# Kernel tuning notes

Measured on AMD Instinct MI355X. Metric: run time of the kernel, lower is better.

The kernel has to match this reference:

```python
import jax, jax.numpy as jnp
import numpy as np

NH, NKV, HD = 32, 8, 128   # query heads, kv heads, head_dim
EPS = 1e-6
ROPE_BASE = 10000.0


def setup_inputs() -> dict:
    key = jax.random.key(0)
    ks = jax.random.split(key, 5)
    B, S, H = 2, 1024, 4096
    scale = 0.02
    return {
        "x": jax.random.normal(ks[0], (B, S, H), jnp.float32),
        "wq": jax.random.normal(ks[1], (H, NH * HD), jnp.float32) * scale,
        "wk": jax.random.normal(ks[2], (H, NKV * HD), jnp.float32) * scale,
        "wv": jax.random.normal(ks[3], (H, NKV * HD), jnp.float32) * scale,
        "wo": jax.random.normal(ks[4], (NH * HD, H), jnp.float32) * scale,
        "q_norm_w": jnp.ones((HD,), jnp.float32),
        "k_norm_w": jnp.ones((HD,), jnp.float32),
    }


def _rmsnorm(t, w):
    # per-head RMSNorm over last dim (head_dim)
    var = jnp.mean(t * t, axis=-1, keepdims=True)
    return t * jax.lax.rsqrt(var + EPS) * w


def _rope(t, cos, sin):
    # t: [B,S,h,d]; cos/sin: [S, d/2] (neox / rotate-half style)
    d2 = t.shape[-1] // 2
    t1, t2 = t[..., :d2], t[..., d2:]
    c = cos[None, :, None, :]
    s = sin[None, :, None, :]
    return jnp.concatenate([t1 * c - t2 * s, t1 * s + t2 * c], axis=-1)


def reference(x, wq, wk, wv, wo, q_norm_w, k_norm_w):
    B, S, H = x.shape
    softmax_scale = HD ** (-0.5)

    q = (x @ wq).reshape(B, S, NH, HD)
    k = (x @ wk).reshape(B, S, NKV, HD)
    v = (x @ wv).reshape(B, S, NKV, HD)

    # QK RMSNorm (qwen3 use_qk_norm)
    q = _rmsnorm(q, q_norm_w)
    k = _rmsnorm(k, k_norm_w)

    # rotary embedding, base 10000
    inv_freq = 1.0 / (ROPE_BASE ** (jnp.arange(0, HD, 2, dtype=jnp.float32) / HD))
    ang = jnp.arange(S, dtype=jnp.float32)[:, None] * inv_freq[None, :]  # [S, d/2]
    cos, sin = jnp.cos(ang), jnp.sin(ang)
    q = _rope(q, cos, sin)
    k = _rope(k, cos, sin)

    # GQA: expand kv heads to match query heads
    g = NH // NKV
    k = jnp.repeat(k, g, axis=2)  # [B,S,NH,HD]
    v = jnp.repeat(v, g, axis=2)

    scores = jnp.einsum("bqhd,bkhd->bhqk", q, k) * softmax_scale
    causal = jnp.tril(jnp.ones((S, S), dtype=bool))
    scores = jnp.where(causal[None, None], scores, jnp.finfo(scores.dtype).min)
    probs = jax.nn.softmax(scores, axis=-1)
    ctx = jnp.einsum("bhqk,bkhd->bqhd", probs, v).reshape(B, S, NH * HD)
    return ctx @ wo
```

## Files before the change

kernel.cpp:

```cpp
#include <hip/hip_runtime.h>


#define NH_ 32
#define NKV_ 8
#define HD_ 128
#define SEQ_ 1024
#define HID_ 4096
#define NQKV_ 6144

typedef unsigned short u16;
typedef __bf16 bf16x8 __attribute__((ext_vector_type(8)));
typedef float f32x4 __attribute__((ext_vector_type(4)));

__device__ __forceinline__ u16 f2bf(float f) {
  unsigned int u = __float_as_uint(f);
  return (u16)((u + 0x7FFFu + ((u >> 16) & 1u)) >> 16);
}
__device__ __forceinline__ float bf2f(u16 u) {
  return __uint_as_float(((unsigned int)u) << 16);
}
__device__ __forceinline__ f32x4 mfma16(bf16x8 a, bf16x8 b, f32x4 c) {
  return __builtin_amdgcn_mfma_f32_16x16x32_bf16(a, b, c, 0, 0, 0);
}
__device__ __forceinline__ void gld16(u16* lds, const u16* g) {
  __builtin_amdgcn_global_load_lds(
      (const __attribute__((address_space(1))) unsigned int*)g,
      (__attribute__((address_space(3))) unsigned int*)lds, 16, 0, 0);
}

__global__ __launch_bounds__(256) void cvt_bf16(const float* __restrict__ src,
                                                u16* __restrict__ dst) {
  int i = (blockIdx.x * 256 + threadIdx.x) * 8;
  float4 a = *(const float4*)(src + i);
  float4 b = *(const float4*)(src + i + 4);
  u16 o[8];
  o[0] = f2bf(a.x); o[1] = f2bf(a.y); o[2] = f2bf(a.z); o[3] = f2bf(a.w);
  o[4] = f2bf(b.x); o[5] = f2bf(b.y); o[6] = f2bf(b.z); o[7] = f2bf(b.w);
  *(uint4*)(dst + i) = *(uint4*)&o[0];
}

__global__ __launch_bounds__(256) void transpose_cvt(
    const float* __restrict__ src, int ldn, u16* __restrict__ dst, int K) {
  __shared__ float t[32][33];
  const int k0 = blockIdx.x * 32, n0 = blockIdx.y * 32;
  const int c = threadIdx.x & 31, r4 = threadIdx.x >> 5;
#pragma unroll
  for (int i = 0; i < 4; ++i) {
    int r = r4 + i * 8;
    t[r][c] = src[(size_t)(k0 + r) * ldn + n0 + c];
  }
  __syncthreads();
#pragma unroll
  for (int i = 0; i < 4; ++i) {
    int r = r4 + i * 8;
    dst[(size_t)(n0 + r) * K + k0 + c] = f2bf(t[c][r]);
  }
}

__global__ __launch_bounds__(256) void v_transpose(const u16* __restrict__ QKV,
                                                   u16* __restrict__ VT) {
  __shared__ u16 t[32][33];
  const int s0 = blockIdx.x * 32, d0 = blockIdx.y * 32;
  const int bkvh = blockIdx.z;
  const int b = bkvh >> 3, kvh = bkvh & 7;
  const int c = threadIdx.x & 31, r8 = threadIdx.x >> 5;
#pragma unroll
  for (int i = 0; i < 4; ++i) {
    int r = r8 + i * 8;
    t[r][c] = QKV[(size_t)(b * SEQ_ + s0 + r) * NQKV_ + 5120 + kvh * 128 + d0 + c];
  }
  __syncthreads();
#pragma unroll
  for (int i = 0; i < 4; ++i) {
    int r = r8 + i * 8;
    VT[(size_t)(bkvh * HD_ + d0 + r) * SEQ_ + s0 + c] = t[c][r];
  }
}

template <bool F32OUT>
__global__ __launch_bounds__(256) void gemm_bt(const u16* __restrict__ A,
                                               const u16* __restrict__ Bt,
                                               void* __restrict__ Cv, int K,
                                               int ldc) {
  __shared__ u16 As[128 * 32];
  __shared__ u16 Bs[128 * 32];
  const int bn = blockIdx.x, bm = blockIdx.y;
  const int tid = threadIdx.x, lane = tid & 63, w = tid >> 6;
  const int wr = w >> 1, wc = w & 1, ln = lane & 15, quad = lane >> 4;

  const int srow = w * 32 + (lane >> 2);
  const int skk = (lane & 3) * 8;
  const u16* ag = A + (size_t)(bm * 128 + srow) * K + skk;
  const u16* bg = Bt + (size_t)(bn * 128 + srow) * K + skk;
  u16* asd = &As[w * 1024];
  u16* bsd = &Bs[w * 1024];

  f32x4 acc[4][4];
#pragma unroll
  for (int i = 0; i < 4; ++i)
#pragma unroll
    for (int j = 0; j < 4; ++j)
#pragma unroll
      for (int r = 0; r < 4; ++r) acc[i][j][r] = 0.0f;

  for (int kb = 0; kb < K / 32; ++kb) {
    gld16(asd, ag);
    gld16(asd + 512, ag + 16 * (size_t)K);
    gld16(bsd, bg);
    gld16(bsd + 512, bg + 16 * (size_t)K);
    ag += 32;
    bg += 32;
    __syncthreads();
    bf16x8 af[4], bfr[4];
#pragma unroll
    for (int i = 0; i < 4; ++i)
      af[i] = *(const bf16x8*)&As[(wr * 64 + i * 16 + ln) * 32 + quad * 8];
#pragma unroll
    for (int j = 0; j < 4; ++j)
      bfr[j] = *(const bf16x8*)&Bs[(wc * 64 + j * 16 + ln) * 32 + quad * 8];
#pragma unroll
    for (int i = 0; i < 4; ++i)
#pragma unroll
      for (int j = 0; j < 4; ++j) acc[i][j] = mfma16(af[i], bfr[j], acc[i][j]);
    __syncthreads();
  }
#pragma unroll
  for (int i = 0; i < 4; ++i) {
#pragma unroll
    for (int r = 0; r < 4; ++r) {
      int grow = bm * 128 + wr * 64 + i * 16 + quad * 4 + r;
      int gcol = bn * 128 + wc * 64 + ln;
      if (F32OUT) {
        float* dst = (float*)Cv + (size_t)grow * ldc + gcol;
#pragma unroll
        for (int j = 0; j < 4; ++j) dst[j * 16] = acc[i][j][r];
      } else {
        u16* dst = (u16*)Cv + (size_t)grow * ldc + gcol;
#pragma unroll
        for (int j = 0; j < 4; ++j) dst[j * 16] = f2bf(acc[i][j][r]);
      }
    }
  }
}

__global__ __launch_bounds__(256) void norm_rope(
    const u16* __restrict__ QKV, const float* __restrict__ QW,
    const float* __restrict__ KW, u16* __restrict__ QB, u16* __restrict__ KB) {
  const float QSCALE = 0.08838834764831845f * 1.4426950408889634f;
  int vec = blockIdx.x * 4 + (threadIdx.x >> 6);
  int lane = threadIdx.x & 63;
  const u16* src;
  u16* dst;
  const float* nw;
  int m;
  float outsc;
  if (vec < 65536) {
    m = vec >> 5;
    int hh = vec & 31;
    src = QKV + (size_t)m * NQKV_ + hh * 128;
    int b = m >> 10, s = m & 1023;
    dst = QB + (size_t)((b * NH_ + hh) * SEQ_ + s) * HD_;
    nw = QW;
    outsc = QSCALE;
  } else {
    int vk = vec - 65536;
    m = vk >> 3;
    int kvh = vk & 7;
    src = QKV + (size_t)m * NQKV_ + 4096 + kvh * 128;
    int b = m >> 10, s = m & 1023;
    dst = KB + (size_t)((b * NKV_ + kvh) * SEQ_ + s) * HD_;
    nw = KW;
    outsc = 1.0f;
  }
  float t1 = bf2f(src[lane]), t2 = bf2f(src[lane + 64]);
  float ss = t1 * t1 + t2 * t2;
#pragma unroll
  for (int off = 32; off >= 1; off >>= 1) ss += __shfl_xor(ss, off);
  float scale = rsqrtf(ss * (1.0f / 128.0f) + 1e-6f) * outsc;
  float n1 = t1 * scale * nw[lane];
  float n2 = t2 * scale * nw[lane + 64];
  int spos = m & 1023;
  float invf = powf(10000.0f, -(float)lane * (1.0f / 64.0f));
  float ang = (float)spos * invf;
  float sn, cs;
  sincosf(ang, &sn, &cs);
  dst[lane] = f2bf(n1 * cs - n2 * sn);
  dst[lane + 64] = f2bf(n1 * sn + n2 * cs);
}

__global__ __launch_bounds__(256) void flash_attn(
    const u16* __restrict__ QB, const u16* __restrict__ KB,
    const u16* __restrict__ VT, u16* __restrict__ CTX) {
  __shared__ u16 Ks[4][64][32];
  __shared__ u16 Vs[2][128][32];
  __shared__ u16 Pl[4][16][72];

  const int bid = blockIdx.x;
  const int qt = 15 - (bid >> 6);
  const int h = bid & 31, b = (bid >> 5) & 1;
  const int kvh = h >> 2;
  const int tid = threadIdx.x, w = tid >> 6, lane = tid & 63;
  const int ln = lane & 15, quad = lane >> 4;
  const int l4 = lane >> 2, l4r = lane & 3;

  const u16* qbase =
      QB + (size_t)((b * NH_ + h) * SEQ_ + qt * 64 + w * 16 + ln) * HD_;
  bf16x8 qf[4];
#pragma unroll
  for (int kc = 0; kc < 4; ++kc)
    qf[kc] = *(const bf16x8*)(qbase + kc * 32 + quad * 8);

  f32x4 o[8];
#pragma unroll
  for (int t = 0; t < 8; ++t)
#pragma unroll
    for (int r = 0; r < 4; ++r) o[t][r] = 0.0f;
  float m_r[4] = {-3e38f, -3e38f, -3e38f, -3e38f};
  float l_r[4] = {0.0f, 0.0f, 0.0f, 0.0f};

  const u16* krow = KB + (size_t)((b * NKV_ + kvh) * SEQ_ + w * 16 + l4) * HD_ +
                    l4r * 8;
  const u16* vrow = VT + (size_t)((b * NKV_ + kvh) * HD_ + w * 32 + l4) * SEQ_ +
                    l4r * 8;
  const int pswz = ((ln >> 3) & 1) << 3;

  for (int kt = 0; kt <= qt; ++kt) {
    const int key0 = kt * 64;
#pragma unroll
    for (int i = 0; i < 4; ++i)
      gld16(&Ks[i][w * 16][0], krow + (size_t)key0 * HD_ + i * 32);
#pragma unroll
    for (int i = 0; i < 4; ++i)
      gld16(&Vs[i & 1][w * 32 + (i >> 1) * 16][0],
            vrow + (size_t)(i >> 1) * 16 * SEQ_ + key0 + (i & 1) * 32);
    __syncthreads();

    f32x4 sc[4];
#pragma unroll
    for (int t2 = 0; t2 < 4; ++t2) {
#pragma unroll
      for (int r = 0; r < 4; ++r) sc[t2][r] = 0.0f;
#pragma unroll
      for (int kc = 0; kc < 4; ++kc) {
        bf16x8 kf = *(const bf16x8*)&Ks[kc][t2 * 16 + ln][quad * 8];
        sc[t2] = mfma16(qf[kc], kf, sc[t2]);
      }
    }

    const bool diag = (kt == qt);
    float p[4][4], alpha[4];
#pragma unroll
    for (int r = 0; r < 4; ++r) {
      float s0 = sc[0][r], s1 = sc[1][r], s2 = sc[2][r], s3 = sc[3][r];
      if (diag) {
        const int qi = qt * 64 + w * 16 + quad * 4 + r;
        if (key0 + ln > qi) s0 = -3e38f;
        if (key0 + 16 + ln > qi) s1 = -3e38f;
        if (key0 + 32 + ln > qi) s2 = -3e38f;
        if (key0 + 48 + ln > qi) s3 = -3e38f;
      }
      float mx = fmaxf(fmaxf(s0, s1), fmaxf(s2, s3));
#pragma unroll
      for (int off = 1; off < 16; off <<= 1) mx = fmaxf(mx, __shfl_xor(mx, off));
      float mnew = fmaxf(m_r[r], mx);
      alpha[r] = exp2f(m_r[r] - mnew);
      p[0][r] = exp2f(s0 - mnew);
      p[1][r] = exp2f(s1 - mnew);
      p[2][r] = exp2f(s2 - mnew);
      p[3][r] = exp2f(s3 - mnew);
      float rs = p[0][r] + p[1][r] + p[2][r] + p[3][r];
#pragma unroll
      for (int off = 1; off < 16; off <<= 1) rs += __shfl_xor(rs, off);
      l_r[r] = l_r[r] * alpha[r] + rs;
      m_r[r] = mnew;
    }
#pragma unroll
    for (int t = 0; t < 8; ++t)
#pragma unroll
      for (int r = 0; r < 4; ++r) o[t][r] *= alpha[r];

#pragma unroll
    for (int r = 0; r < 4; ++r) {
      const int row = quad * 4 + r;
      const int wswz = ((row >> 3) & 1) << 3;
#pragma unroll
      for (int t2 = 0; t2 < 4; ++t2)
        Pl[w][row][(t2 * 16 + ln) ^ wswz] = f2bf(p[t2][r]);
    }
    bf16x8 af0 = *(const bf16x8*)&Pl[w][ln][(quad * 8) ^ pswz];
    bf16x8 af1 = *(const bf16x8*)&Pl[w][ln][32 + ((quad * 8) ^ pswz)];
#pragma unroll
    for (int t = 0; t < 8; ++t) {
      bf16x8 vf0 = *(const bf16x8*)&Vs[0][t * 16 + ln][quad * 8];
      o[t] = mfma16(af0, vf0, o[t]);
      bf16x8 vf1 = *(const bf16x8*)&Vs[1][t * 16 + ln][quad * 8];
      o[t] = mfma16(af1, vf1, o[t]);
    }
    __syncthreads();
  }

#pragma unroll
  for (int r = 0; r < 4; ++r) {
    float inv_l = 1.0f / l_r[r];
    int srow = qt * 64 + w * 16 + quad * 4 + r;
    u16* dst = CTX + (size_t)(b * SEQ_ + srow) * (NH_ * HD_) + h * HD_;
#pragma unroll
    for (int t = 0; t < 8; ++t) dst[t * 16 + ln] = f2bf(o[t][r] * inv_l);
  }
}

extern "C" void kernel_launch(void* const* d_in, const int* in_sizes, int n_in,
                              void* d_out, int out_size, void* d_ws,
                              size_t ws_size, hipStream_t stream) {
  const float* x = (const float*)d_in[0];
  const float* wq = (const float*)d_in[1];
  const float* wk = (const float*)d_in[2];
  const float* wv = (const float*)d_in[3];
  const float* wo = (const float*)d_in[4];
  const float* qw = (const float*)d_in[5];
  const float* kw = (const float*)d_in[6];
  float* out = (float*)d_out;
  char* ws = (char*)d_ws;
  const size_t MB = 1024 * 1024;

  u16* wqkvt = (u16*)ws;
  u16* wot = (u16*)ws;
  u16* xb = (u16*)(ws + 48 * MB);
  u16* qkv = (u16*)(ws + 64 * MB);
  u16* ctx = (u16*)(ws + 64 * MB);
  u16* qb = (u16*)(ws + 88 * MB);
  u16* kb = (u16*)(ws + 104 * MB);
  u16* vt = (u16*)(ws + 108 * MB);

  cvt_bf16<<<dim3(4096), 256, 0, stream>>>(x, xb);
  transpose_cvt<<<dim3(128, 128), 256, 0, stream>>>(wq, 4096, wqkvt, 4096);
  transpose_cvt<<<dim3(128, 32), 256, 0, stream>>>(
      wk, 1024, wqkvt + (size_t)4096 * 4096, 4096);
  transpose_cvt<<<dim3(128, 32), 256, 0, stream>>>(
      wv, 1024, wqkvt + (size_t)5120 * 4096, 4096);
  gemm_bt<false><<<dim3(48, 16), 256, 0, stream>>>(xb, wqkvt, qkv, 4096, 6144);
  transpose_cvt<<<dim3(128, 128), 256, 0, stream>>>(wo, 4096, wot, 4096);
  norm_rope<<<dim3(20480), 256, 0, stream>>>(qkv, qw, kw, qb, kb);
  v_transpose<<<dim3(32, 4, 16), 256, 0, stream>>>(qkv, vt);
  flash_attn<<<dim3(1024), 256, 0, stream>>>(qb, kb, vt, ctx);
  gemm_bt<true><<<dim3(32, 16), 256, 0, stream>>>(ctx, wot, out, 4096, 4096);
}
```

Baseline: 542.8 us.

## Double-buffer flash attention K/V tiles with 128-row query blocks; fuse QKV weight transposes

The flash attention kernel now gives each block 128 query rows, each wave handling two 16-row tiles, so every K/V tile loaded to LDS is reused twice. K/V tiles are double-buffered so the next tile's global loads are issued before the current tile is computed. Waves whose rows lie entirely before a key tile skip that tile. The three Q/K/V weight transpose launches are merged into one kernel. The costs are fewer blocks (512), more registers and LDS per block, and some load imbalance across waves on causal tiles.

```diff
diff --git a/kernel.cpp b/kernel.cpp
--- a/kernel.cpp
+++ b/kernel.cpp
@@ -54,6 +54,32 @@
   for (int i = 0; i < 4; ++i) {
     int r = r4 + i * 8;
     dst[(size_t)(n0 + r) * K + k0 + c] = f2bf(t[c][r]);
+  }
+}
+
+__global__ __launch_bounds__(256) void transpose_cvt3(
+    const float* __restrict__ wq, const float* __restrict__ wk,
+    const float* __restrict__ wv, u16* __restrict__ dst) {
+  __shared__ float t[32][33];
+  const int k0 = blockIdx.x * 32;
+  const int y = blockIdx.y;
+  const float* src;
+  int ldn, n0;
+  size_t dofs;
+  if (y < 128) { src = wq; ldn = 4096; n0 = y * 32; dofs = 0; }
+  else if (y < 160) { src = wk; ldn = 1024; n0 = (y - 128) * 32; dofs = (size_t)4096 * 4096; }
+  else { src = wv; ldn = 1024; n0 = (y - 160) * 32; dofs = (size_t)5120 * 4096; }
+  const int c = threadIdx.x & 31, r4 = threadIdx.x >> 5;
+#pragma unroll
+  for (int i = 0; i < 4; ++i) {
+    int r = r4 + i * 8;
+    t[r][c] = src[(size_t)(k0 + r) * ldn + n0 + c];
+  }
+  __syncthreads();
+#pragma unroll
+  for (int i = 0; i < 4; ++i) {
+    int r = r4 + i * 8;
+    dst[dofs + (size_t)(n0 + r) * HID_ + k0 + c] = f2bf(t[c][r]);
   }
 }
 
@@ -188,125 +214,151 @@
   dst[lane + 64] = f2bf(n1 * sn + n2 * cs);
 }
 
-__global__ __launch_bounds__(256) void flash_attn(
+__global__ __launch_bounds__(256, 2) void flash_attn(
     const u16* __restrict__ QB, const u16* __restrict__ KB,
     const u16* __restrict__ VT, u16* __restrict__ CTX) {
-  __shared__ u16 Ks[4][64][32];
-  __shared__ u16 Vs[2][128][32];
+  __shared__ u16 Ks[2][4][64][32];
+  __shared__ u16 Vs[2][2][128][32];
   __shared__ u16 Pl[4][16][72];
 
   const int bid = blockIdx.x;
-  const int qt = 15 - (bid >> 6);
+  const int qt = 7 - (bid >> 6);
   const int h = bid & 31, b = (bid >> 5) & 1;
   const int kvh = h >> 2;
   const int tid = threadIdx.x, w = tid >> 6, lane = tid & 63;
   const int ln = lane & 15, quad = lane >> 4;
-  const int l4 = lane >> 2, l4r = lane & 3;
-
-  const u16* qbase =
-      QB + (size_t)((b * NH_ + h) * SEQ_ + qt * 64 + w * 16 + ln) * HD_;
-  bf16x8 qf[4];
-#pragma unroll
-  for (int kc = 0; kc < 4; ++kc)
-    qf[kc] = *(const bf16x8*)(qbase + kc * 32 + quad * 8);
-
-  f32x4 o[8];
-#pragma unroll
-  for (int t = 0; t < 8; ++t)
-#pragma unroll
-    for (int r = 0; r < 4; ++r) o[t][r] = 0.0f;
-  float m_r[4] = {-3e38f, -3e38f, -3e38f, -3e38f};
-  float l_r[4] = {0.0f, 0.0f, 0.0f, 0.0f};
-
-  const u16* krow = KB + (size_t)((b * NKV_ + kvh) * SEQ_ + w * 16 + l4) * HD_ +
-                    l4r * 8;
-  const u16* vrow = VT + (size_t)((b * NKV_ + kvh) * HD_ + w * 32 + l4) * SEQ_ +
-                    l4r * 8;
+
+  const u16* qbase = QB + (size_t)((b * NH_ + h) * SEQ_ + qt * 128) * HD_;
+  bf16x8 qf[2][4];
+#pragma unroll
+  for (int rt = 0; rt < 2; ++rt)
+#pragma unroll
+    for (int kc = 0; kc < 4; ++kc)
+      qf[rt][kc] = *(const bf16x8*)(qbase +
+                                    (size_t)(w * 32 + rt * 16 + ln) * HD_ +
+                                    kc * 32 + quad * 8);
+
+  f32x4 o[2][8];
+#pragma unroll
+  for (int rt = 0; rt < 2; ++rt)
+#pragma unroll
+    for (int t = 0; t < 8; ++t)
+#pragma unroll
+      for (int r = 0; r < 4; ++r) o[rt][t][r] = 0.0f;
+  float m_r[2][4] = {{-3e38f, -3e38f, -3e38f, -3e38f},
+                     {-3e38f, -3e38f, -3e38f, -3e38f}};
+  float l_r[2][4] = {{0, 0, 0, 0}, {0, 0, 0, 0}};
+
+  const u16* krow = KB + (size_t)((b * NKV_ + kvh) * SEQ_ + w * 16 + (lane >> 2)) * HD_ +
+                    (lane & 3) * 8;
+  const u16* vrow = VT + (size_t)((b * NKV_ + kvh) * HD_ + w * 32 + (lane >> 2)) * SEQ_ +
+                    (lane & 3) * 8;
   const int pswz = ((ln >> 3) & 1) << 3;
-
-  for (int kt = 0; kt <= qt; ++kt) {
+  const int nkt = 2 * qt + 2;
+  const int wave_max_row = qt * 128 + w * 32 + 31;
+
+#pragma unroll
+  for (int i = 0; i < 4; ++i) gld16(&Ks[0][i][w * 16][0], krow + i * 32);
+#pragma unroll
+  for (int i = 0; i < 4; ++i)
+    gld16(&Vs[0][i & 1][w * 32 + (i >> 1) * 16][0],
+          vrow + (size_t)(i >> 1) * 16 * SEQ_ + (i & 1) * 32);
+
+  for (int kt = 0; kt < nkt; ++kt) {
     const int key0 = kt * 64;
-#pragma unroll
-    for (int i = 0; i < 4; ++i)
-      gld16(&Ks[i][w * 16][0], krow + (size_t)key0 * HD_ + i * 32);
-#pragma unroll
-    for (int i = 0; i < 4; ++i)
-      gld16(&Vs[i & 1][w * 32 + (i >> 1) * 16][0],
-            vrow + (size_t)(i >> 1) * 16 * SEQ_ + key0 + (i & 1) * 32);
+    const int buf = kt & 1;
     __syncthreads();
 
-    f32x4 sc[4];
-#pragma unroll
-    for (int t2 = 0; t2 < 4; ++t2) {
-#pragma unroll
-      for (int r = 0; r < 4; ++r) sc[t2][r] = 0.0f;
-#pragma unroll
-      for (int kc = 0; kc < 4; ++kc) {
-        bf16x8 kf = *(const bf16x8*)&Ks[kc][t2 * 16 + ln][quad * 8];
-        sc[t2] = mfma16(qf[kc], kf, sc[t2]);
-      }
+    if (kt + 1 < nkt) {
+      const int nk0 = key0 + 64, nbuf = buf ^ 1;
+#pragma unroll
+      for (int i = 0; i < 4; ++i)
+        gld16(&Ks[nbuf][i][w * 16][0], krow + (size_t)nk0 * HD_ + i * 32);
+#pragma unroll
+      for (int i = 0; i < 4; ++i)
+        gld16(&Vs[nbuf][i & 1][w * 32 + (i >> 1) * 16][0],
+              vrow + (size_t)(i >> 1) * 16 * SEQ_ + nk0 + (i & 1) * 32);
     }
 
-    const bool diag = (kt == qt);
-    float p[4][4], alpha[4];
+    if (key0 > wave_max_row) continue;
+    const bool diag = (kt >= 2 * qt);
+
+#pragma unroll
+    for (int rt = 0; rt < 2; ++rt) {
+      f32x4 sc[4];
+#pragma unroll
+      for (int t2 = 0; t2 < 4; ++t2) {
+#pragma unroll
+        for (int r = 0; r < 4; ++r) sc[t2][r] = 0.0f;
+#pragma unroll
+        for (int kc = 0; kc < 4; ++kc) {
+          bf16x8 kf = *(const bf16x8*)&Ks[buf][kc][t2 * 16 + ln][quad * 8];
+          sc[t2] = mfma16(qf[rt][kc], kf, sc[t2]);
+        }
+      }
+
+      float p[4][4], alpha[4];
+#pragma unroll
+      for (int r = 0; r < 4; ++r) {
+        float s0 = sc[0][r], s1 = sc[1][r], s2 = sc[2][r], s3 = sc[3][r];
+        if (diag) {
+          const int qi = qt * 128 + w * 32 + rt * 16 + quad * 4 + r;
+          if (key0 + ln > qi) s0 = -3e38f;
+          if (key0 + 16 + ln > qi) s1 = -3e38f;
+          if (key0 + 32 + ln > qi) s2 = -3e38f;
+          if (key0 + 48 + ln > qi) s3 = -3e38f;
+        }
+        float mx = fmaxf(fmaxf(s0, s1), fmaxf(s2, s3));
+#pragma unroll
+        for (int off = 1; off < 16; off <<= 1)
+          mx = fmaxf(mx, __shfl_xor(mx, off));
+        float mnew = fmaxf(m_r[rt][r], mx);
+        alpha[r] = exp2f(m_r[rt][r] - mnew);
+        p[0][r] = exp2f(s0 - mnew);
+        p[1][r] = exp2f(s1 - mnew);
+        p[2][r] = exp2f(s2 - mnew);
+        p[3][r] = exp2f(s3 - mnew);
+        float rs = p[0][r] + p[1][r] + p[2][r] + p[3][r];
+#pragma unroll
+        for (int off = 1; off < 16; off <<= 1) rs += __shfl_xor(rs, off);
+        l_r[rt][r] = l_r[rt][r] * alpha[r] + rs;
+        m_r[rt][r] = mnew;
+      }
+#pragma unroll
+      for (int t = 0; t < 8; ++t)
+#pragma unroll
+        for (int r = 0; r < 4; ++r) o[rt][t][r] *= alpha[r];
+
+#pragma unroll
+      for (int r = 0; r < 4; ++r) {
+        const int row = quad * 4 + r;
+        const int wswz = ((row >> 3) & 1) << 3;
+#pragma unroll
+        for (int t2 = 0; t2 < 4; ++t2)
+          Pl[w][row][(t2 * 16 + ln) ^ wswz] = f2bf(p[t2][r]);
+      }
+      bf16x8 af0 = *(const bf16x8*)&Pl[w][ln][(quad * 8) ^ pswz];
+      bf16x8 af1 = *(const bf16x8*)&Pl[w][ln][32 + ((quad * 8) ^ pswz)];
+#pragma unroll
+      for (int t = 0; t < 8; ++t) {
+        bf16x8 vf0 = *(const bf16x8*)&Vs[buf][0][t * 16 + ln][quad * 8];
+        o[rt][t] = mfma16(af0, vf0, o[rt][t]);
+        bf16x8 vf1 = *(const bf16x8*)&Vs[buf][1][t * 16 + ln][quad * 8];
+        o[rt][t] = mfma16(af1, vf1, o[rt][t]);
+      }
+    }
+  }
+
+#pragma unroll
+  for (int rt = 0; rt < 2; ++rt)
 #pragma unroll
     for (int r = 0; r < 4; ++r) {
-      float s0 = sc[0][r], s1 = sc[1][r], s2 = sc[2][r], s3 = sc[3][r];
-      if (diag) {
-        const int qi = qt * 64 + w * 16 + quad * 4 + r;
-        if (key0 + ln > qi) s0 = -3e38f;
-        if (key0 + 16 + ln > qi) s1 = -3e38f;
-        if (key0 + 32 + ln > qi) s2 = -3e38f;
-        if (key0 + 48 + ln > qi) s3 = -3e38f;
-      }
-      float mx = fmaxf(fmaxf(s0, s1), fmaxf(s2, s3));
-#pragma unroll
-      for (int off = 1; off < 16; off <<= 1) mx = fmaxf(mx, __shfl_xor(mx, off));
-      float mnew = fmaxf(m_r[r], mx);
-      alpha[r] = exp2f(m_r[r] - mnew);
-      p[0][r] = exp2f(s0 - mnew);
-      p[1][r] = exp2f(s1 - mnew);
-      p[2][r] = exp2f(s2 - mnew);
-      p[3][r] = exp2f(s3 - mnew);
-      float rs = p[0][r] + p[1][r] + p[2][r] + p[3][r];
-#pragma unroll
-      for (int off = 1; off < 16; off <<= 1) rs += __shfl_xor(rs, off);
-      l_r[r] = l_r[r] * alpha[r] + rs;
-      m_r[r] = mnew;
+      float inv_l = 1.0f / l_r[rt][r];
+      int srow = qt * 128 + w * 32 + rt * 16 + quad * 4 + r;
+      u16* dst = CTX + (size_t)(b * SEQ_ + srow) * (NH_ * HD_) + h * HD_;
+#pragma unroll
+      for (int t = 0; t < 8; ++t) dst[t * 16 + ln] = f2bf(o[rt][t][r] * inv_l);
     }
-#pragma unroll
-    for (int t = 0; t < 8; ++t)
-#pragma unroll
-      for (int r = 0; r < 4; ++r) o[t][r] *= alpha[r];
-
-#pragma unroll
-    for (int r = 0; r < 4; ++r) {
-      const int row = quad * 4 + r;
-      const int wswz = ((row >> 3) & 1) << 3;
-#pragma unroll
-      for (int t2 = 0; t2 < 4; ++t2)
-        Pl[w][row][(t2 * 16 + ln) ^ wswz] = f2bf(p[t2][r]);
-    }
-    bf16x8 af0 = *(const bf16x8*)&Pl[w][ln][(quad * 8) ^ pswz];
-    bf16x8 af1 = *(const bf16x8*)&Pl[w][ln][32 + ((quad * 8) ^ pswz)];
-#pragma unroll
-    for (int t = 0; t < 8; ++t) {
-      bf16x8 vf0 = *(const bf16x8*)&Vs[0][t * 16 + ln][quad * 8];
-      o[t] = mfma16(af0, vf0, o[t]);
-      bf16x8 vf1 = *(const bf16x8*)&Vs[1][t * 16 + ln][quad * 8];
-      o[t] = mfma16(af1, vf1, o[t]);
-    }
-    __syncthreads();
-  }
-
-#pragma unroll
-  for (int r = 0; r < 4; ++r) {
-    float inv_l = 1.0f / l_r[r];
-    int srow = qt * 64 + w * 16 + quad * 4 + r;
-    u16* dst = CTX + (size_t)(b * SEQ_ + srow) * (NH_ * HD_) + h * HD_;
-#pragma unroll
-    for (int t = 0; t < 8; ++t) dst[t * 16 + ln] = f2bf(o[t][r] * inv_l);
-  }
 }
 
 extern "C" void kernel_launch(void* const* d_in, const int* in_sizes, int n_in,
@@ -333,15 +385,11 @@
   u16* vt = (u16*)(ws + 108 * MB);
 
   cvt_bf16<<<dim3(4096), 256, 0, stream>>>(x, xb);
-  transpose_cvt<<<dim3(128, 128), 256, 0, stream>>>(wq, 4096, wqkvt, 4096);
-  transpose_cvt<<<dim3(128, 32), 256, 0, stream>>>(
-      wk, 1024, wqkvt + (size_t)4096 * 4096, 4096);
-  transpose_cvt<<<dim3(128, 32), 256, 0, stream>>>(
-      wv, 1024, wqkvt + (size_t)5120 * 4096, 4096);
+  transpose_cvt3<<<dim3(128, 192), 256, 0, stream>>>(wq, wk, wv, wqkvt);
   gemm_bt<false><<<dim3(48, 16), 256, 0, stream>>>(xb, wqkvt, qkv, 4096, 6144);
   transpose_cvt<<<dim3(128, 128), 256, 0, stream>>>(wo, 4096, wot, 4096);
   norm_rope<<<dim3(20480), 256, 0, stream>>>(qkv, qw, kw, qb, kb);
   v_transpose<<<dim3(32, 4, 16), 256, 0, stream>>>(qkv, vt);
-  flash_attn<<<dim3(1024), 256, 0, stream>>>(qb, kb, vt, ctx);
+  flash_attn<<<dim3(512), 256, 0, stream>>>(qb, kb, vt, ctx);
   gemm_bt<true><<<dim3(32, 16), 256, 0, stream>>>(ctx, wot, out, 4096, 4096);
 }
```

Measured after the change: 564.7 us. 4.0% more time.
